# Kernel tuning notes

Measured on AMD Instinct MI355X. Metric: run time of the kernel, lower is better.

## Reference

```python
import jax, jax.numpy as jnp
import numpy as np

MAT_MODE = [(0, 1), (0, 2), (1, 2)]   # plane axes per component (TensoRF VM)
VEC_MODE = [2, 1, 0]                  # line axis per component
DISTANCE_SCALE = 1.0
WHITE_BG = True


def _bilinear(plane, uv):
    """plane: [C,H,W]; uv: [P,2] in [-1,1] (uv[:,0]->W, uv[:,1]->H). align_corners=True."""
    H, W = plane.shape[-2], plane.shape[-1]
    x = (uv[:, 0] + 1.0) * 0.5 * (W - 1)
    y = (uv[:, 1] + 1.0) * 0.5 * (H - 1)
    x0 = jnp.clip(jnp.floor(x), 0, W - 2).astype(jnp.int32)
    y0 = jnp.clip(jnp.floor(y), 0, H - 2).astype(jnp.int32)
    wx = x - x0
    wy = y - y0
    v00 = plane[:, y0, x0]
    v01 = plane[:, y0, x0 + 1]
    v10 = plane[:, y0 + 1, x0]
    v11 = plane[:, y0 + 1, x0 + 1]
    top = v00 * (1 - wx) + v01 * wx
    bot = v10 * (1 - wx) + v11 * wx
    return top * (1 - wy) + bot * wy   # [C,P]


def _linear1d(line, t):
    """line: [C,L]; t: [P] in [-1,1]. align_corners=True."""
    L = line.shape[-1]
    x = (t + 1.0) * 0.5 * (L - 1)
    x0 = jnp.clip(jnp.floor(x), 0, L - 2).astype(jnp.int32)
    w = x - x0
    return line[:, x0] * (1 - w) + line[:, x0 + 1] * w   # [C,P]


def setup_inputs() -> dict:
    key = jax.random.key(0)
    ks = jax.random.split(key, 8)
    N_rays = 4096
    # camera origins on a sphere of radius 4, dirs aimed at points inside the box
    o = jax.random.normal(ks[0], (N_rays, 3), jnp.float32)
    o = o / jnp.linalg.norm(o, axis=-1, keepdims=True) * 4.0
    tgt = jax.random.uniform(ks[1], (N_rays, 3), jnp.float32, -0.5, 0.5)
    d = tgt - o
    d = d / jnp.linalg.norm(d, axis=-1, keepdims=True)
    rays = jnp.concatenate([o, d], axis=-1)
    return {
        "rays": rays,
        "density_plane": 0.1 * jax.random.normal(ks[2], (3, 16, 256, 256), jnp.float32),
        "density_line": 0.1 * jax.random.normal(ks[3], (3, 16, 256), jnp.float32),
        "app_plane": 0.1 * jax.random.normal(ks[4], (3, 24, 256, 256), jnp.float32),
        "app_line": 0.1 * jax.random.normal(ks[5], (3, 24, 256), jnp.float32),
        "basis_mat": 0.1 * jax.random.normal(ks[6], (72, 3), jnp.float32),
        "aabb": jnp.array([[-1.5, -1.5, -1.5], [1.5, 1.5, 1.5]], jnp.float32),
        "N_samples": 256,
    }


def reference(rays, density_plane, density_line, app_plane, app_line, basis_mat, aabb, N_samples):
    N = rays.shape[0]
    o, d = rays[:, :3], rays[:, 3:6]
    # ray / aabb intersection
    vec = jnp.where(jnp.abs(d) < 1e-6, 1e-6, d)
    rate_a = (aabb[1] - o) / vec
    rate_b = (aabb[0] - o) / vec
    t_min = jnp.clip(jnp.minimum(rate_a, rate_b).max(-1), 0.05)
    t_max = jnp.maximum(jnp.maximum(rate_a, rate_b).min(-1), t_min + 1e-3)
    s = jnp.linspace(0.0, 1.0, N_samples, dtype=jnp.float32)
    z = t_min[:, None] * (1.0 - s) + t_max[:, None] * s          # [N,S]
    dists = jnp.diff(z, axis=-1)
    dists = jnp.concatenate([dists, dists[:, -1:]], axis=-1)      # [N,S]
    pts = o[:, None, :] + d[:, None, :] * z[..., None]            # [N,S,3]
    coords = (pts - aabb[0]) / (aabb[1] - aabb[0]) * 2.0 - 1.0
    inside = jnp.all(jnp.abs(coords) <= 1.0, axis=-1)             # [N,S]
    cf = coords.reshape(-1, 3)                                    # [P,3]

    sigma_feat = 0.0
    app_feats = []
    for i in range(3):
        uv = cf[:, list(MAT_MODE[i])]
        w = cf[:, VEC_MODE[i]]
        sigma_feat = sigma_feat + (_bilinear(density_plane[i], uv) * _linear1d(density_line[i], w)).sum(0)
        app_feats.append(_bilinear(app_plane[i], uv) * _linear1d(app_line[i], w))
    app = jnp.concatenate(app_feats, axis=0).T                    # [P, 72]

    sigma = jax.nn.softplus(sigma_feat).reshape(N, -1) * inside   # [N,S]
    alpha = 1.0 - jnp.exp(-sigma * dists * DISTANCE_SCALE)        # [N,S]
    T = jnp.cumprod(1.0 - alpha + 1e-10, axis=-1)
    T = jnp.concatenate([jnp.ones_like(T[:, :1]), T[:, :-1]], axis=-1)
    weights = alpha * T                                           # [N,S]

    rgb = jax.nn.sigmoid(app @ basis_mat).reshape(N, -1, 3)       # [N,S,3]
    rgb_map = (weights[..., None] * rgb).sum(1)                   # [N,3]
    acc = weights.sum(-1)
    if WHITE_BG:
        rgb_map = rgb_map + (1.0 - acc)[..., None]
    rgb_map = jnp.clip(rgb_map, 0.0, 1.0)
    depth_map = (weights * z).sum(-1, keepdims=True)              # [N,1]
    return rgb_map, depth_map
```

## Files before the change

### kernel.cpp

```cpp
#include <hip/hip_runtime.h>
#include <hip/hip_fp16.h>
#include <cmath>

#define NRAYS 4096
#define NSAMP 256
#define NSAMPLES_TOT (NRAYS * NSAMP)

static constexpr size_t DPT_B = 0;
static constexpr size_t DLT_B = 3145728;
static constexpr size_t APT_B = DLT_B + 24576;
static constexpr size_t ALT_B = APT_B + 6291456;
static constexpr size_t SMP_B = ALT_B + 24576;
static constexpr size_t RAY_B = SMP_B + 8388608;
static constexpr size_t WS_NEED = RAY_B + 131072;

typedef _Float16 __attribute__((ext_vector_type(2))) v2h;
typedef __attribute__((ext_vector_type(2))) float f32x2;

#if defined(__has_builtin)
#if __has_builtin(__builtin_amdgcn_cvt_scalef32_pk_f16_fp8)
#define HAS_SCVT 1
#endif
#endif
#ifndef HAS_SCVT
#define HAS_SCVT 0
#endif

__device__ __forceinline__ float dot2acc(__half2 a, __half2 b, float c) {
  return __builtin_amdgcn_fdot2(__builtin_bit_cast(v2h, a),
                                __builtin_bit_cast(v2h, b), c, false);
}

__device__ __forceinline__ __half2 lerp2(__half2 a, __half2 b, __half2 w) {
  return __hfma2(w, __hsub2(b, a), a);
}

__device__ __forceinline__ void ld8h(const __half* p, __half2 h[4]) {
  uint4 r = *(const uint4*)p;
  h[0] = __builtin_bit_cast(__half2, r.x);
  h[1] = __builtin_bit_cast(__half2, r.y);
  h[2] = __builtin_bit_cast(__half2, r.z);
  h[3] = __builtin_bit_cast(__half2, r.w);
}

__device__ __forceinline__ unsigned pack2h(float a, float b) {
  return __builtin_bit_cast(unsigned, __floats2half2_rn(a, b));
}

__device__ __forceinline__ void dec4f8h(unsigned w, __half2& h0, __half2& h1) {
#if HAS_SCVT
  v2h a = __builtin_amdgcn_cvt_scalef32_pk_f16_fp8((int)w, 1.0f, false);
  v2h b = __builtin_amdgcn_cvt_scalef32_pk_f16_fp8((int)w, 1.0f, true);
  h0 = __builtin_bit_cast(__half2, a);
  h1 = __builtin_bit_cast(__half2, b);
#else
  f32x2 lo = __builtin_amdgcn_cvt_pk_f32_fp8((int)w, false);
  f32x2 hi = __builtin_amdgcn_cvt_pk_f32_fp8((int)w, true);
  h0 = __floats2half2_rn(lo.x, lo.y);
  h1 = __floats2half2_rn(hi.x, hi.y);
#endif
}

__device__ __forceinline__ void dec8f8(uint2 q, __half2 h[4]) {
  dec4f8h(q.x, h[0], h[1]);
  dec4f8h(q.y, h[2], h[3]);
}

__device__ __forceinline__ void dec16f8(uint4 q, __half2 h[8]) {
  dec4f8h(q.x, h[0], h[1]);
  dec4f8h(q.y, h[2], h[3]);
  dec4f8h(q.z, h[4], h[5]);
  dec4f8h(q.w, h[6], h[7]);
}

__device__ __forceinline__ unsigned pk4f8(float a, float b, float c, float d) {
  int w = __builtin_amdgcn_cvt_pk_fp8_f32(a, b, 0, false);
  w = __builtin_amdgcn_cvt_pk_fp8_f32(c, d, w, true);
  return (unsigned)w;
}

__device__ __forceinline__ void grid_uv(float c, int& i0, float& w) {
  float f = (c + 1.0f) * 127.5f;
  float fl = floorf(f);
  fl = fminf(fmaxf(fl, 0.0f), 254.0f);
  i0 = (int)fl;
  w = f - fl;
}

__device__ __forceinline__ void bilin_w(float wx, float wy, __half2& W00,
                                        __half2& W01, __half2& W10, __half2& W11) {
  float ix = 1.0f - wx, iy = 1.0f - wy;
  W00 = __float2half2_rn(ix * iy);
  W01 = __float2half2_rn(wx * iy);
  W10 = __float2half2_rn(ix * wy);
  W11 = __float2half2_rn(wx * wy);
}

__global__ __launch_bounds__(256) void prep_kernel(
    const float* __restrict__ dp, const float* __restrict__ ap,
    const float* __restrict__ dl, const float* __restrict__ al,
    const float* __restrict__ rays, const float* __restrict__ aabb,
    unsigned char* __restrict__ dpt, unsigned char* __restrict__ apt,
    __half* __restrict__ dlt, unsigned char* __restrict__ alt,
    float4* __restrict__ rd) {
  __shared__ float tile[24][257];
  int b = blockIdx.x, x = threadIdx.x;
  if (b < 768) {
    int i = b >> 8, y = b & 255;
    const float* src = dp + (size_t)(i * 16) * 65536 + y * 256;
#pragma unroll
    for (int c = 0; c < 16; ++c) tile[c][x] = src[c * 65536 + x];
    __syncthreads();
    float f[16];
#pragma unroll
    for (int c = 0; c < 16; ++c) f[c] = tile[c][x];
    uint4 v;
    v.x = pk4f8(f[0], f[1], f[2], f[3]);
    v.y = pk4f8(f[4], f[5], f[6], f[7]);
    v.z = pk4f8(f[8], f[9], f[10], f[11]);
    v.w = pk4f8(f[12], f[13], f[14], f[15]);
    *(uint4*)(dpt + ((size_t)(i << 16) + (y << 8) + x) * 16) = v;
  } else if (b < 1536) {
    int t = b - 768;
    int i = t >> 8, y = t & 255;
    const float* src = ap + (size_t)(i * 24) * 65536 + y * 256;
#pragma unroll
    for (int c = 0; c < 24; ++c) tile[c][x] = src[c * 65536 + x];
    __syncthreads();
    float f[24];
#pragma unroll
    for (int c = 0; c < 24; ++c) f[c] = tile[c][x];
    uint4 v0, v1;
    v0.x = pk4f8(f[0], f[1], f[2], f[3]);
    v0.y = pk4f8(f[4], f[5], f[6], f[7]);
    v0.z = pk4f8(f[8], f[9], f[10], f[11]);
    v0.w = pk4f8(f[12], f[13], f[14], f[15]);
    v1.x = pk4f8(f[16], f[17], f[18], f[19]);
    v1.y = pk4f8(f[20], f[21], f[22], f[23]);
    v1.z = 0u; v1.w = 0u;
    uint4* dst = (uint4*)(apt + ((size_t)(i << 16) + (y << 8) + x) * 32);
    dst[0] = v0; dst[1] = v1;
  } else if (b < 1539) {
    int i = b - 1536, l = x;
    float f[16];
#pragma unroll
    for (int c = 0; c < 16; ++c) f[c] = dl[(i * 16 + c) * 256 + l];
    uint4 v0, v1;
    v0.x = pack2h(f[0], f[1]);   v0.y = pack2h(f[2], f[3]);
    v0.z = pack2h(f[4], f[5]);   v0.w = pack2h(f[6], f[7]);
    v1.x = pack2h(f[8], f[9]);   v1.y = pack2h(f[10], f[11]);
    v1.z = pack2h(f[12], f[13]); v1.w = pack2h(f[14], f[15]);
    uint4* dst = (uint4*)(dlt + (i * 256 + l) * 16);
    dst[0] = v0; dst[1] = v1;
  } else if (b < 1542) {
    int i = b - 1539, l = x;
    float f[24];
#pragma unroll
    for (int c = 0; c < 24; ++c) f[c] = al[(i * 24 + c) * 256 + l];
    uint4 v0, v1;
    v0.x = pk4f8(f[0], f[1], f[2], f[3]);
    v0.y = pk4f8(f[4], f[5], f[6], f[7]);
    v0.z = pk4f8(f[8], f[9], f[10], f[11]);
    v0.w = pk4f8(f[12], f[13], f[14], f[15]);
    v1.x = pk4f8(f[16], f[17], f[18], f[19]);
    v1.y = pk4f8(f[20], f[21], f[22], f[23]);
    v1.z = 0u; v1.w = 0u;
    uint4* dst = (uint4*)(alt + (i * 256 + l) * 32);
    dst[0] = v0; dst[1] = v1;
  } else {
    int r = (b - 1542) * 256 + x;
    if (r < NRAYS) {
      float o0 = rays[r * 6 + 0], o1 = rays[r * 6 + 1], o2 = rays[r * 6 + 2];
      float d0 = rays[r * 6 + 3], d1 = rays[r * 6 + 4], d2 = rays[r * 6 + 5];
      float A0 = aabb[0], A1 = aabb[1], A2 = aabb[2];
      float B0 = aabb[3], B1 = aabb[4], B2 = aabb[5];
      float v0 = fabsf(d0) < 1e-6f ? 1e-6f : d0;
      float v1 = fabsf(d1) < 1e-6f ? 1e-6f : d1;
      float v2 = fabsf(d2) < 1e-6f ? 1e-6f : d2;
      float ra0 = (B0 - o0) / v0, rb0 = (A0 - o0) / v0;
      float ra1 = (B1 - o1) / v1, rb1 = (A1 - o1) / v1;
      float ra2 = (B2 - o2) / v2, rb2 = (A2 - o2) / v2;
      float tmin = fmaxf(fmaxf(fminf(ra0, rb0), fminf(ra1, rb1)), fminf(ra2, rb2));
      tmin = fmaxf(tmin, 0.05f);
      float tmax = fminf(fminf(fmaxf(ra0, rb0), fmaxf(ra1, rb1)), fmaxf(ra2, rb2));
      tmax = fmaxf(tmax, tmin + 0.001f);
      float dt = (tmax - tmin) * (1.0f / 255.0f);
      float s0 = 2.0f / (B0 - A0), s1 = 2.0f / (B1 - A1), s2 = 2.0f / (B2 - A2);
      float4 a2, b2;
      a2.x = (o0 - A0) * s0 - 1.0f; a2.y = (o1 - A1) * s1 - 1.0f;
      a2.z = (o2 - A2) * s2 - 1.0f; a2.w = tmin;
      b2.x = d0 * s0; b2.y = d1 * s1; b2.z = d2 * s2; b2.w = dt;
      rd[r * 2] = a2;
      rd[r * 2 + 1] = b2;
    }
  }
}

__device__ __forceinline__ float density_f8(const unsigned char* __restrict__ pl,
                                            const __half* __restrict__ ln,
                                            int x0, int y0, int l0,
                                            __half2 W00, __half2 W01,
                                            __half2 W10, __half2 W11,
                                            __half2 wl, int sub, float acc) {
  const unsigned char* p = pl + (size_t)((y0 * 256 + x0) << 4) + sub * 8;
  uint2 q00 = *(const uint2*)p;
  uint2 q01 = *(const uint2*)(p + 16);
  uint2 q10 = *(const uint2*)(p + 4096);
  uint2 q11 = *(const uint2*)(p + 4096 + 16);
  __half2 A[4], B[4], C[4], D[4], la[4], lb[4];
  dec8f8(q00, A); dec8f8(q01, B); dec8f8(q10, C); dec8f8(q11, D);
  const __half* lp = ln + (l0 << 4) + sub * 8;
  ld8h(lp, la); ld8h(lp + 16, lb);
#pragma unroll
  for (int r = 0; r < 4; ++r) {
    __half2 m = __hmul2(W00, A[r]);
    m = __hfma2(W01, B[r], m);
    m = __hfma2(W10, C[r], m);
    m = __hfma2(W11, D[r], m);
    __half2 l = lerp2(la[r], lb[r], wl);
    acc = dot2acc(m, l, acc);
  }
  return acc;
}

__device__ __forceinline__ void app_f8(const unsigned char* __restrict__ pl,
                                       const unsigned char* __restrict__ ln,
                                       const __half2* __restrict__ btR,
                                       const __half2* __restrict__ btG,
                                       const __half2* __restrict__ btB,
                                       int x0, int y0, int l0,
                                       __half2 W00, __half2 W01,
                                       __half2 W10, __half2 W11,
                                       __half2 wl, int sub,
                                       float& dr, float& dg, float& db) {
  const unsigned char* p = pl + ((size_t)(y0 * 256 + x0) << 5) + sub * 16;
  uint4 qA = *(const uint4*)p;
  uint4 qB = *(const uint4*)(p + 32);
  uint4 qC = *(const uint4*)(p + 8192);
  uint4 qD = *(const uint4*)(p + 8192 + 32);
  const unsigned char* lp = ln + (l0 << 5) + sub * 16;
  uint4 qLA = *(const uint4*)lp;
  uint4 qLB = *(const uint4*)(lp + 32);
  __half2 A[8], B[8], C[8], D[8], LA[8], LB[8];
  dec16f8(qA, A); dec16f8(qB, B); dec16f8(qC, C); dec16f8(qD, D);
  dec16f8(qLA, LA); dec16f8(qLB, LB);
#pragma unroll
  for (int r = 0; r < 8; ++r) {
    __half2 m = __hmul2(W00, A[r]);
    m = __hfma2(W01, B[r], m);
    m = __hfma2(W10, C[r], m);
    m = __hfma2(W11, D[r], m);
    __half2 l = lerp2(LA[r], LB[r], wl);
    __half2 av = __hmul2(m, l);
    dr = dot2acc(av, btR[r], dr);
    dg = dot2acc(av, btG[r], dg);
    db = dot2acc(av, btB[r], db);
  }
}

__global__ __launch_bounds__(256) void sample_kernel(
    const float4* __restrict__ rd, const float* __restrict__ basis,
    const unsigned char* __restrict__ dpt, const __half* __restrict__ dlt,
    const unsigned char* __restrict__ apt, const unsigned char* __restrict__ alt,
    uint2* __restrict__ smp) {
  __shared__ __align__(16) __half bth[3][3][32];
  int tid = threadIdx.x;
  for (int t = tid; t < 288; t += 256) {
    int k = t / 96, rem = t - k * 96;
    int m = rem >> 5, c = rem & 31;
    float v = (c < 24) ? basis[(m * 24 + c) * 3 + k] : 0.0f;
    bth[k][m][c] = __float2half(v);
  }
  __syncthreads();

  int ray = blockIdx.x >> 1;
  int j = ((blockIdx.x & 1) << 7) + (tid >> 1);
  int sub = tid & 1;

  float4 ra = rd[ray * 2];
  float4 rb = rd[ray * 2 + 1];
  float z = fmaf((float)j, rb.w, ra.w);
  float c0 = fmaf(rb.x, z, ra.x);
  float c1 = fmaf(rb.y, z, ra.y);
  float c2 = fmaf(rb.z, z, ra.z);
  bool inside = (fabsf(c0) <= 1.0f) && (fabsf(c1) <= 1.0f) && (fabsf(c2) <= 1.0f);

  float sig = 0.f, dr = 0.f, dg = 0.f, db = 0.f;
  if (inside) {
    int i0, i1, i2;
    float w0, w1, w2;
    grid_uv(c0, i0, w0);
    grid_uv(c1, i1, w1);
    grid_uv(c2, i2, w2);
    __half2 h0 = __float2half2_rn(w0);
    __half2 h1 = __float2half2_rn(w1);
    __half2 h2 = __float2half2_rn(w2);
    __half2 Wa00, Wa01, Wa10, Wa11;
    __half2 Wb00, Wb01, Wb10, Wb11;
    __half2 Wc00, Wc01, Wc10, Wc11;
    bilin_w(w0, w1, Wa00, Wa01, Wa10, Wa11);
    bilin_w(w0, w2, Wb00, Wb01, Wb10, Wb11);
    bilin_w(w1, w2, Wc00, Wc01, Wc10, Wc11);

    sig = density_f8(dpt + 0 * 1048576, dlt + 0 * 4096, i0, i1, i2,
                     Wa00, Wa01, Wa10, Wa11, h2, sub, sig);
    sig = density_f8(dpt + 1 * 1048576, dlt + 1 * 4096, i0, i2, i1,
                     Wb00, Wb01, Wb10, Wb11, h1, sub, sig);
    sig = density_f8(dpt + 2 * 1048576, dlt + 2 * 4096, i1, i2, i0,
                     Wc00, Wc01, Wc10, Wc11, h0, sub, sig);
    app_f8(apt + 0 * 2097152, alt + 0 * 8192,
           (const __half2*)&bth[0][0][sub * 16], (const __half2*)&bth[1][0][sub * 16],
           (const __half2*)&bth[2][0][sub * 16], i0, i1, i2,
           Wa00, Wa01, Wa10, Wa11, h2, sub, dr, dg, db);
    app_f8(apt + 1 * 2097152, alt + 1 * 8192,
           (const __half2*)&bth[0][1][sub * 16], (const __half2*)&bth[1][1][sub * 16],
           (const __half2*)&bth[2][1][sub * 16], i0, i2, i1,
           Wb00, Wb01, Wb10, Wb11, h1, sub, dr, dg, db);
    app_f8(apt + 2 * 2097152, alt + 2 * 8192,
           (const __half2*)&bth[0][2][sub * 16], (const __half2*)&bth[1][2][sub * 16],
           (const __half2*)&bth[2][2][sub * 16], i1, i2, i0,
           Wc00, Wc01, Wc10, Wc11, h0, sub, dr, dg, db);
  }
  sig += __shfl_xor(sig, 1, 64);
  dr += __shfl_xor(dr, 1, 64);
  dg += __shfl_xor(dg, 1, 64);
  db += __shfl_xor(db, 1, 64);

  if (sub == 0) {
    float e = __expf(-fabsf(sig));
    float sp = fmaxf(sig, 0.f) + __logf(1.0f + e);
    float alpha = inside ? (1.0f - __expf(-sp * rb.w)) : 0.0f;
    float cr = __builtin_amdgcn_rcpf(1.0f + __expf(-dr));
    float cg = __builtin_amdgcn_rcpf(1.0f + __expf(-dg));
    float cb = __builtin_amdgcn_rcpf(1.0f + __expf(-db));
    uint2 sv;
    sv.x = pack2h(alpha, cr);
    sv.y = pack2h(cg, cb);
    smp[ray * 256 + j] = sv;
  }
}

__global__ __launch_bounds__(256) void scan_kernel(
    const float4* __restrict__ rd, const uint2* __restrict__ smp,
    float* __restrict__ out) {
  int tid = threadIdx.x;
  int lane = tid & 63;
  int ray = blockIdx.x * 4 + (tid >> 6);

  float tmin = rd[ray * 2].w;
  float dt = rd[ray * 2 + 1].w;

  float C = 1.0f;
  float racc = 0.f, gacc = 0.f, bacc = 0.f, wsum = 0.f, dsum = 0.f;

  for (int q = 0; q < 4; ++q) {
    int j = q * 64 + lane;
    uint2 sv = smp[ray * 256 + j];
    float2 ar = __half22float2(__builtin_bit_cast(__half2, sv.x));
    float2 gb = __half22float2(__builtin_bit_cast(__half2, sv.y));
    float alpha = ar.x;
    float z = fmaf((float)j, dt, tmin);

    float p = 1.0f - alpha + 1e-10f;
#pragma unroll
    for (int off = 1; off < 64; off <<= 1) {
      float t = __shfl_up(p, off, 64);
      if (lane >= off) p *= t;
    }
    float tot = __shfl(p, 63, 64);
    float e = __shfl_up(p, 1, 64);
    if (lane == 0) e = 1.0f;
    float Tj = C * e;
    float w = alpha * Tj;
    racc += w * ar.y;
    gacc += w * gb.x;
    bacc += w * gb.y;
    wsum += w;
    dsum += w * z;
    C *= tot;
  }

#pragma unroll
  for (int off = 32; off > 0; off >>= 1) {
    racc += __shfl_down(racc, off, 64);
    gacc += __shfl_down(gacc, off, 64);
    bacc += __shfl_down(bacc, off, 64);
    wsum += __shfl_down(wsum, off, 64);
    dsum += __shfl_down(dsum, off, 64);
  }
  if (lane == 0) {
    float bgw = 1.0f - wsum;
    out[ray * 3 + 0] = fminf(fmaxf(racc + bgw, 0.f), 1.f);
    out[ray * 3 + 1] = fminf(fmaxf(gacc + bgw, 0.f), 1.f);
    out[ray * 3 + 2] = fminf(fmaxf(bacc + bgw, 0.f), 1.f);
    out[NRAYS * 3 + ray] = dsum;
  }
}

__device__ __forceinline__ float density_orig(const float* __restrict__ plane,
                                              const float* __restrict__ line,
                                              float cx, float cy, float cw) {
  int x0, y0, l0; float wx, wy, wl;
  grid_uv(cx, x0, wx); grid_uv(cy, y0, wy); grid_uv(cw, l0, wl);
  int base = y0 * 256 + x0;
  float s = 0.0f;
#pragma unroll 4
  for (int c = 0; c < 16; ++c) {
    const float* pc = plane + c * 65536;
    float v00 = pc[base], v01 = pc[base + 1];
    float v10 = pc[base + 256], v11 = pc[base + 257];
    float top = fmaf(wx, v01 - v00, v00);
    float bot = fmaf(wx, v11 - v10, v10);
    float mid = fmaf(wy, bot - top, top);
    float la = line[c * 256 + l0], lb = line[c * 256 + l0 + 1];
    float lv = fmaf(wl, lb - la, la);
    s += mid * lv;
  }
  return s;
}

__device__ __forceinline__ void app_orig(const float* __restrict__ plane,
                                         const float* __restrict__ line,
                                         const float* __restrict__ btR,
                                         const float* __restrict__ btG,
                                         const float* __restrict__ btB,
                                         float cx, float cy, float cw,
                                         float& dr, float& dg, float& db) {
  int x0, y0, l0; float wx, wy, wl;
  grid_uv(cx, x0, wx); grid_uv(cy, y0, wy); grid_uv(cw, l0, wl);
  int base = y0 * 256 + x0;
#pragma unroll 4
  for (int c = 0; c < 24; ++c) {
    const float* pc = plane + c * 65536;
    float v00 = pc[base], v01 = pc[base + 1];
    float v10 = pc[base + 256], v11 = pc[base + 257];
    float top = fmaf(wx, v01 - v00, v00);
    float bot = fmaf(wx, v11 - v10, v10);
    float mid = fmaf(wy, bot - top, top);
    float la = line[c * 256 + l0], lb = line[c * 256 + l0 + 1];
    float lv = fmaf(wl, lb - la, la);
    float av = mid * lv;
    dr += av * btR[c]; dg += av * btG[c]; db += av * btB[c];
  }
}

__global__ __launch_bounds__(256) void render_fallback(
    const float* __restrict__ rays, const float* __restrict__ basis,
    const float* __restrict__ aabb, const float* __restrict__ dplane,
    const float* __restrict__ dline, const float* __restrict__ aplane,
    const float* __restrict__ aline, float* __restrict__ out) {
  __shared__ float bt[3 * 72];
  int tid = threadIdx.x;
  if (tid < 216) {
    int k = tid / 72, r = tid - k * 72;
    bt[tid] = basis[r * 3 + k];
  }
  __syncthreads();
  int lane = tid & 63;
  int ray = blockIdx.x * 4 + (tid >> 6);

  float o0 = rays[ray * 6 + 0], o1 = rays[ray * 6 + 1], o2 = rays[ray * 6 + 2];
  float d0 = rays[ray * 6 + 3], d1 = rays[ray * 6 + 4], d2 = rays[ray * 6 + 5];
  float A0 = aabb[0], A1 = aabb[1], A2 = aabb[2];
  float B0 = aabb[3], B1 = aabb[4], B2 = aabb[5];
  float v0 = fabsf(d0) < 1e-6f ? 1e-6f : d0;
  float v1 = fabsf(d1) < 1e-6f ? 1e-6f : d1;
  float v2 = fabsf(d2) < 1e-6f ? 1e-6f : d2;
  float ra0 = (B0 - o0) / v0, rb0 = (A0 - o0) / v0;
  float ra1 = (B1 - o1) / v1, rb1 = (A1 - o1) / v1;
  float ra2 = (B2 - o2) / v2, rb2 = (A2 - o2) / v2;
  float tmin = fmaxf(fmaxf(fminf(ra0, rb0), fminf(ra1, rb1)), fminf(ra2, rb2));
  tmin = fmaxf(tmin, 0.05f);
  float tmax = fminf(fminf(fmaxf(ra0, rb0), fmaxf(ra1, rb1)), fmaxf(ra2, rb2));
  tmax = fmaxf(tmax, tmin + 0.001f);
  float dt = (tmax - tmin) * (1.0f / 255.0f);
  float s0 = 2.0f / (B0 - A0), s1 = 2.0f / (B1 - A1), s2 = 2.0f / (B2 - A2);

  float C = 1.0f;
  float racc = 0.f, gacc = 0.f, bacc = 0.f, wsum = 0.f, dsum = 0.f;
  for (int q = 0; q < 4; ++q) {
    int j = q * 64 + lane;
    float sfrac = (float)j * (1.0f / 255.0f);
    float z = tmin * (1.0f - sfrac) + tmax * sfrac;
    float c0 = (o0 + d0 * z - A0) * s0 - 1.0f;
    float c1 = (o1 + d1 * z - A1) * s1 - 1.0f;
    float c2 = (o2 + d2 * z - A2) * s2 - 1.0f;
    bool inside = (fabsf(c0) <= 1.0f) && (fabsf(c1) <= 1.0f) && (fabsf(c2) <= 1.0f);
    float alpha = 0.f, cr = 0.f, cg = 0.f, cb = 0.f;
    if (inside) {
      float sig = 0.f, dr = 0.f, dg = 0.f, db = 0.f;
      sig += density_orig(dplane + 0 * 1048576, dline + 0 * 4096, c0, c1, c2);
      sig += density_orig(dplane + 1 * 1048576, dline + 1 * 4096, c0, c2, c1);
      sig += density_orig(dplane + 2 * 1048576, dline + 2 * 4096, c1, c2, c0);
      app_orig(aplane + 0 * 1572864, aline + 0 * 6144,
               &bt[0 * 72 + 0], &bt[1 * 72 + 0], &bt[2 * 72 + 0],
               c0, c1, c2, dr, dg, db);
      app_orig(aplane + 1 * 1572864, aline + 1 * 6144,
               &bt[0 * 72 + 24], &bt[1 * 72 + 24], &bt[2 * 72 + 24],
               c0, c2, c1, dr, dg, db);
      app_orig(aplane + 2 * 1572864, aline + 2 * 6144,
               &bt[0 * 72 + 48], &bt[1 * 72 + 48], &bt[2 * 72 + 48],
               c1, c2, c0, dr, dg, db);
      float sp = fmaxf(sig, 0.f) + log1pf(expf(-fabsf(sig)));
      alpha = 1.0f - expf(-sp * dt);
      cr = 1.0f / (1.0f + expf(-dr));
      cg = 1.0f / (1.0f + expf(-dg));
      cb = 1.0f / (1.0f + expf(-db));
    }
    float p = 1.0f - alpha + 1e-10f;
#pragma unroll
    for (int off = 1; off < 64; off <<= 1) {
      float t = __shfl_up(p, off, 64);
      if (lane >= off) p *= t;
    }
    float tot = __shfl(p, 63, 64);
    float e = __shfl_up(p, 1, 64);
    if (lane == 0) e = 1.0f;
    float Tj = C * e;
    float w = alpha * Tj;
    racc += w * cr; gacc += w * cg; bacc += w * cb;
    wsum += w; dsum += w * z;
    C *= tot;
  }
#pragma unroll
  for (int off = 32; off > 0; off >>= 1) {
    racc += __shfl_down(racc, off, 64);
    gacc += __shfl_down(gacc, off, 64);
    bacc += __shfl_down(bacc, off, 64);
    wsum += __shfl_down(wsum, off, 64);
    dsum += __shfl_down(dsum, off, 64);
  }
  if (lane == 0) {
    float bgw = 1.0f - wsum;
    out[ray * 3 + 0] = fminf(fmaxf(racc + bgw, 0.f), 1.f);
    out[ray * 3 + 1] = fminf(fmaxf(gacc + bgw, 0.f), 1.f);
    out[ray * 3 + 2] = fminf(fmaxf(bacc + bgw, 0.f), 1.f);
    out[NRAYS * 3 + ray] = dsum;
  }
}

extern "C" void kernel_launch(void* const* d_in, const int* in_sizes, int n_in,
                              void* d_out, int out_size, void* d_ws, size_t ws_size,
                              hipStream_t stream) {
  const float* rays  = (const float*)d_in[0];
  const float* dp    = (const float*)d_in[1];
  const float* dl    = (const float*)d_in[2];
  const float* ap    = (const float*)d_in[3];
  const float* al    = (const float*)d_in[4];
  const float* basis = (const float*)d_in[5];
  const float* aabb  = (const float*)d_in[6];
  float* out = (float*)d_out;

  if (ws_size >= WS_NEED) {
    char* ws = (char*)d_ws;
    unsigned char* dpt = (unsigned char*)(ws + DPT_B);
    __half* dlt = (__half*)(ws + DLT_B);
    unsigned char* apt = (unsigned char*)(ws + APT_B);
    unsigned char* alt = (unsigned char*)(ws + ALT_B);
    uint2* smp = (uint2*)(ws + SMP_B);
    float4* rayd = (float4*)(ws + RAY_B);
    prep_kernel<<<1558, 256, 0, stream>>>(dp, ap, dl, al, rays, aabb,
                                          dpt, apt, dlt, alt, rayd);
    sample_kernel<<<NRAYS * 2, 256, 0, stream>>>(rayd, basis, dpt, dlt, apt, alt, smp);
    scan_kernel<<<NRAYS / 4, 256, 0, stream>>>(rayd, smp, out);
  } else {
    render_fallback<<<NRAYS / 4, 256, 0, stream>>>(
        rays, basis, aabb, dp, dl, ap, al, out);
  }
}
```

Before: 153.7 us.

## Fuse sample and scan kernels into one per-ray block, drop prep LDS transpose

Merges the per-sample feature kernel and the transmittance scan kernel into a single 512-thread block per ray. Per-sample alpha and colour now go to shared memory instead of a global intermediate buffer, which removes a launch and an 8 MB global write and read-back. The prep kernel also drops its shared-memory tile and syncthreads, reading channels straight from global memory with coalesced loads. In exchange, only one wave per block does the serial scan while the other seven wait, and the block barriers may reduce overlap.

```diff
diff --git a/kernel.cpp b/kernel.cpp
--- a/kernel.cpp
+++ b/kernel.cpp
@@ -4,14 +4,12 @@
 
 #define NRAYS 4096
 #define NSAMP 256
-#define NSAMPLES_TOT (NRAYS * NSAMP)
 
 static constexpr size_t DPT_B = 0;
 static constexpr size_t DLT_B = 3145728;
 static constexpr size_t APT_B = DLT_B + 24576;
 static constexpr size_t ALT_B = APT_B + 6291456;
-static constexpr size_t SMP_B = ALT_B + 24576;
-static constexpr size_t RAY_B = SMP_B + 8388608;
+static constexpr size_t RAY_B = ALT_B + 24576;
 static constexpr size_t WS_NEED = RAY_B + 131072;
 
 typedef _Float16 __attribute__((ext_vector_type(2))) v2h;
@@ -103,17 +101,13 @@
     unsigned char* __restrict__ dpt, unsigned char* __restrict__ apt,
     __half* __restrict__ dlt, unsigned char* __restrict__ alt,
     float4* __restrict__ rd) {
-  __shared__ float tile[24][257];
   int b = blockIdx.x, x = threadIdx.x;
   if (b < 768) {
     int i = b >> 8, y = b & 255;
-    const float* src = dp + (size_t)(i * 16) * 65536 + y * 256;
-#pragma unroll
-    for (int c = 0; c < 16; ++c) tile[c][x] = src[c * 65536 + x];
-    __syncthreads();
+    const float* src = dp + (size_t)(i * 16) * 65536 + y * 256 + x;
     float f[16];
 #pragma unroll
-    for (int c = 0; c < 16; ++c) f[c] = tile[c][x];
+    for (int c = 0; c < 16; ++c) f[c] = src[c * 65536];
     uint4 v;
     v.x = pk4f8(f[0], f[1], f[2], f[3]);
     v.y = pk4f8(f[4], f[5], f[6], f[7]);
@@ -123,13 +117,10 @@
   } else if (b < 1536) {
     int t = b - 768;
     int i = t >> 8, y = t & 255;
-    const float* src = ap + (size_t)(i * 24) * 65536 + y * 256;
-#pragma unroll
-    for (int c = 0; c < 24; ++c) tile[c][x] = src[c * 65536 + x];
-    __syncthreads();
+    const float* src = ap + (size_t)(i * 24) * 65536 + y * 256 + x;
     float f[24];
 #pragma unroll
-    for (int c = 0; c < 24; ++c) f[c] = tile[c][x];
+    for (int c = 0; c < 24; ++c) f[c] = src[c * 65536];
     uint4 v0, v1;
     v0.x = pk4f8(f[0], f[1], f[2], f[3]);
     v0.y = pk4f8(f[4], f[5], f[6], f[7]);
@@ -258,24 +249,23 @@
   }
 }
 
-__global__ __launch_bounds__(256) void sample_kernel(
+__global__ __launch_bounds__(512, 8) void render_fused(
     const float4* __restrict__ rd, const float* __restrict__ basis,
     const unsigned char* __restrict__ dpt, const __half* __restrict__ dlt,
     const unsigned char* __restrict__ apt, const unsigned char* __restrict__ alt,
-    uint2* __restrict__ smp) {
+    float* __restrict__ out) {
   __shared__ __align__(16) __half bth[3][3][32];
+  __shared__ __align__(16) float4 sm[NSAMP];
   int tid = threadIdx.x;
-  for (int t = tid; t < 288; t += 256) {
-    int k = t / 96, rem = t - k * 96;
+  if (tid < 288) {
+    int k = tid / 96, rem = tid - k * 96;
     int m = rem >> 5, c = rem & 31;
     float v = (c < 24) ? basis[(m * 24 + c) * 3 + k] : 0.0f;
     bth[k][m][c] = __float2half(v);
   }
-  __syncthreads();
-
-  int ray = blockIdx.x >> 1;
-  int j = ((blockIdx.x & 1) << 7) + (tid >> 1);
-  int sub = tid & 1;
+
+  int ray = blockIdx.x;
+  int j = tid >> 1, sub = tid & 1;
 
   float4 ra = rd[ray * 2];
   float4 rb = rd[ray * 2 + 1];
@@ -284,6 +274,8 @@
   float c1 = fmaf(rb.y, z, ra.y);
   float c2 = fmaf(rb.z, z, ra.z);
   bool inside = (fabsf(c0) <= 1.0f) && (fabsf(c1) <= 1.0f) && (fabsf(c2) <= 1.0f);
+
+  __syncthreads();
 
   float sig = 0.f, dr = 0.f, dg = 0.f, db = 0.f;
   if (inside) {
@@ -329,71 +321,58 @@
   if (sub == 0) {
     float e = __expf(-fabsf(sig));
     float sp = fmaxf(sig, 0.f) + __logf(1.0f + e);
-    float alpha = inside ? (1.0f - __expf(-sp * rb.w)) : 0.0f;
-    float cr = __builtin_amdgcn_rcpf(1.0f + __expf(-dr));
-    float cg = __builtin_amdgcn_rcpf(1.0f + __expf(-dg));
-    float cb = __builtin_amdgcn_rcpf(1.0f + __expf(-db));
-    uint2 sv;
-    sv.x = pack2h(alpha, cr);
-    sv.y = pack2h(cg, cb);
-    smp[ray * 256 + j] = sv;
-  }
-}
-
-__global__ __launch_bounds__(256) void scan_kernel(
-    const float4* __restrict__ rd, const uint2* __restrict__ smp,
-    float* __restrict__ out) {
-  int tid = threadIdx.x;
-  int lane = tid & 63;
-  int ray = blockIdx.x * 4 + (tid >> 6);
-
-  float tmin = rd[ray * 2].w;
-  float dt = rd[ray * 2 + 1].w;
-
-  float C = 1.0f;
-  float racc = 0.f, gacc = 0.f, bacc = 0.f, wsum = 0.f, dsum = 0.f;
-
-  for (int q = 0; q < 4; ++q) {
-    int j = q * 64 + lane;
-    uint2 sv = smp[ray * 256 + j];
-    float2 ar = __half22float2(__builtin_bit_cast(__half2, sv.x));
-    float2 gb = __half22float2(__builtin_bit_cast(__half2, sv.y));
-    float alpha = ar.x;
-    float z = fmaf((float)j, dt, tmin);
-
-    float p = 1.0f - alpha + 1e-10f;
-#pragma unroll
-    for (int off = 1; off < 64; off <<= 1) {
-      float t = __shfl_up(p, off, 64);
-      if (lane >= off) p *= t;
+    float4 sv;
+    sv.x = inside ? (1.0f - __expf(-sp * rb.w)) : 0.0f;
+    sv.y = __builtin_amdgcn_rcpf(1.0f + __expf(-dr));
+    sv.z = __builtin_amdgcn_rcpf(1.0f + __expf(-dg));
+    sv.w = __builtin_amdgcn_rcpf(1.0f + __expf(-db));
+    sm[j] = sv;
+  }
+  __syncthreads();
+
+  if (tid < 64) {
+    int lane = tid;
+    float tmin = ra.w, dt = rb.w;
+    float C = 1.0f;
+    float racc = 0.f, gacc = 0.f, bacc = 0.f, wsum = 0.f, dsum = 0.f;
+    for (int q = 0; q < 4; ++q) {
+      int jj = q * 64 + lane;
+      float4 sv = sm[jj];
+      float alpha = sv.x;
+      float zz = fmaf((float)jj, dt, tmin);
+      float p = 1.0f - alpha + 1e-10f;
+#pragma unroll
+      for (int off = 1; off < 64; off <<= 1) {
+        float t = __shfl_up(p, off, 64);
+        if (lane >= off) p *= t;
+      }
+      float tot = __shfl(p, 63, 64);
+      float e = __shfl_up(p, 1, 64);
+      if (lane == 0) e = 1.0f;
+      float Tj = C * e;
+      float w = alpha * Tj;
+      racc += w * sv.y;
+      gacc += w * sv.z;
+      bacc += w * sv.w;
+      wsum += w;
+      dsum += w * zz;
+      C *= tot;
     }
-    float tot = __shfl(p, 63, 64);
-    float e = __shfl_up(p, 1, 64);
-    if (lane == 0) e = 1.0f;
-    float Tj = C * e;
-    float w = alpha * Tj;
-    racc += w * ar.y;
-    gacc += w * gb.x;
-    bacc += w * gb.y;
-    wsum += w;
-    dsum += w * z;
-    C *= tot;
-  }
-
-#pragma unroll
-  for (int off = 32; off > 0; off >>= 1) {
-    racc += __shfl_down(racc, off, 64);
-    gacc += __shfl_down(gacc, off, 64);
-    bacc += __shfl_down(bacc, off, 64);
-    wsum += __shfl_down(wsum, off, 64);
-    dsum += __shfl_down(dsum, off, 64);
-  }
-  if (lane == 0) {
-    float bgw = 1.0f - wsum;
-    out[ray * 3 + 0] = fminf(fmaxf(racc + bgw, 0.f), 1.f);
-    out[ray * 3 + 1] = fminf(fmaxf(gacc + bgw, 0.f), 1.f);
-    out[ray * 3 + 2] = fminf(fmaxf(bacc + bgw, 0.f), 1.f);
-    out[NRAYS * 3 + ray] = dsum;
+#pragma unroll
+    for (int off = 32; off > 0; off >>= 1) {
+      racc += __shfl_down(racc, off, 64);
+      gacc += __shfl_down(gacc, off, 64);
+      bacc += __shfl_down(bacc, off, 64);
+      wsum += __shfl_down(wsum, off, 64);
+      dsum += __shfl_down(dsum, off, 64);
+    }
+    if (lane == 0) {
+      float bgw = 1.0f - wsum;
+      out[ray * 3 + 0] = fminf(fmaxf(racc + bgw, 0.f), 1.f);
+      out[ray * 3 + 1] = fminf(fmaxf(gacc + bgw, 0.f), 1.f);
+      out[ray * 3 + 2] = fminf(fmaxf(bacc + bgw, 0.f), 1.f);
+      out[NRAYS * 3 + ray] = dsum;
+    }
   }
 }
 
@@ -557,12 +536,10 @@
     __half* dlt = (__half*)(ws + DLT_B);
     unsigned char* apt = (unsigned char*)(ws + APT_B);
     unsigned char* alt = (unsigned char*)(ws + ALT_B);
-    uint2* smp = (uint2*)(ws + SMP_B);
     float4* rayd = (float4*)(ws + RAY_B);
     prep_kernel<<<1558, 256, 0, stream>>>(dp, ap, dl, al, rays, aabb,
                                           dpt, apt, dlt, alt, rayd);
-    sample_kernel<<<NRAYS * 2, 256, 0, stream>>>(rayd, basis, dpt, dlt, apt, alt, smp);
-    scan_kernel<<<NRAYS / 4, 256, 0, stream>>>(rayd, smp, out);
+    render_fused<<<NRAYS, 512, 0, stream>>>(rayd, basis, dpt, dlt, apt, alt, out);
   } else {
     render_fallback<<<NRAYS / 4, 256, 0, stream>>>(
         rays, basis, aabb, dp, dl, ap, al, out);
```

After: 221.6 us. +44.2%, slower.
